# Optimization experiments

Hardware: AMD Instinct MI355X
Metric: run time of the kernel (lower is better)

The kernel has to match this reference:

```python
import jax, jax.numpy as jnp
import numpy as np

T, B, E = 2048, 16, 1024   # time, batch, embed_dim (fairseq T x B x C layout)
CDIM = 1024                # conv_dim
H = 16                     # num_heads
K = 31                     # kernel_size, padding_l = K-1 (causal left pad)


def _xavier(k, shape):
    fan_out, fan_in = shape
    lim = float(np.sqrt(6.0 / (fan_in + fan_out)))
    return jax.random.uniform(k, shape, jnp.float32, -lim, lim)


def setup_inputs() -> dict:
    key = jax.random.key(0)
    ks = jax.random.split(key, 5)
    return {
        "x": jax.random.normal(ks[0], (T, B, E), jnp.float32),
        "w1": _xavier(ks[1], (CDIM, E)),
        "b1": jnp.zeros((CDIM,), jnp.float32),
        "ww": _xavier(ks[2], (H * K, CDIM)),  # DynamicConv weight_linear
        "bw": jnp.zeros((H * K,), jnp.float32),
        "w2": _xavier(ks[3], (E, CDIM)),
        "b2": jnp.zeros((E,), jnp.float32),
        "gamma": jnp.ones((E,), jnp.float32),
        "beta": jnp.zeros((E,), jnp.float32),
    }


def layer_norm(x, g, b, eps=1e-5):
    m = x.mean(-1, keepdims=True)
    v = ((x - m) ** 2).mean(-1, keepdims=True)
    return (x - m) * jax.lax.rsqrt(v + eps) * g + b


def dynamic_conv(h, ww, bw):
    # h: [T, B, C]; per-position softmax kernel weights shared across R=C/H channels per head
    Tn, Bn, C = h.shape
    R = C // H
    w = jax.nn.softmax((h @ ww.T + bw).reshape(Tn, Bn, H, K), axis=-1)  # [T,B,H,K]
    hp = jnp.pad(h.reshape(Tn, Bn, H, R), ((K - 1, 0), (0, 0), (0, 0), (0, 0)))
    # out[t] = sum_k w[t,:,:,k] * h[t + k - (K-1)]  (causal banded aggregation)
    acc = jnp.zeros((Tn, Bn, H, R), h.dtype)
    for k in range(K):  # fixed small kernel-size loop, not a data-dim loop
        acc = acc + w[:, :, :, k:k + 1] * hp[k:k + Tn]
    return acc.reshape(Tn, Bn, C)


def reference(x, w1, b1, ww, bw, w2, b2, gamma, beta):
    # eval mode: all dropouts are identity; normalize_before=False -> LN after residual
    h = x @ w1.T + b1            # linear1: [T,B,E] -> [T,B,CDIM]
    h = dynamic_conv(h, ww, bw)  # DynamicConv, weight_softmax=True, no conv bias
    h = h @ w2.T + b2            # linear2: back to embed_dim
    return layer_norm(x + h, gamma, beta)
```

## Files before the change

### kernel.cpp

```cpp
#include <hip/hip_runtime.h>

#define T_DIM 2048
#define B_DIM 16
#define E_DIM 1024
#define CD    1024
#define NH    16
#define KSZ   31
#define M_DIM 32768
#define SLICE 131072
#define BSTRIDE 2097152

typedef unsigned int u32;
typedef unsigned short u16;
typedef __attribute__((ext_vector_type(8))) __bf16 bf16x8;
typedef __attribute__((ext_vector_type(4))) float f32x4;
typedef __attribute__((ext_vector_type(4))) float fvec4;
typedef __attribute__((ext_vector_type(8))) unsigned short us8;
typedef __attribute__((ext_vector_type(4))) unsigned short us4;
typedef __attribute__((ext_vector_type(4))) unsigned int ui4;

__device__ __forceinline__ float bf2f(u16 u) {
  union { float f; u32 i; } c; c.i = ((u32)u) << 16; return c.f;
}
__device__ __forceinline__ u16 f2bf(float f) {
  union { float f; u32 i; } c; c.f = f;
  u32 u = c.i;
  u += 0x7fffu + ((u >> 16) & 1u);
  return (u16)(u >> 16);
}

#define GLDS(gp, lp)                                                        \
  __builtin_amdgcn_global_load_lds(                                         \
      (__attribute__((address_space(1))) void*)(gp),                        \
      (__attribute__((address_space(3))) void*)(lp), 16, 0, 0)

__global__ __launch_bounds__(256) void zfill(u16* __restrict__ z) {
  ((ui4*)z)[threadIdx.x] = (ui4)(0u);
}

__global__ __launch_bounds__(256) void cvt_f32_bf16(const float* __restrict__ src,
                                                    u16* __restrict__ dst, int n4) {
  int i = blockIdx.x * 256 + threadIdx.x;
  int stride = gridDim.x * 256;
  const fvec4* s4 = (const fvec4*)src;
  us4* d4 = (us4*)dst;
  for (; i < n4; i += stride) {
    fvec4 v = s4[i];
    us4 o;
    o[0] = f2bf(v[0]); o[1] = f2bf(v[1]); o[2] = f2bf(v[2]); o[3] = f2bf(v[3]);
    d4[i] = o;
  }
}

__global__ __launch_bounds__(256) void cvt_x_tr(const float* __restrict__ x,
                                                u16* __restrict__ xbt) {
  int rr = blockIdx.x;
  int t = rr >> 4, b = rr & 15;
  const fvec4* src = (const fvec4*)(x + (size_t)rr * E_DIM);
  us4* dst = (us4*)(xbt + ((size_t)b * T_DIM + t) * E_DIM);
  fvec4 v = src[threadIdx.x];
  us4 o;
  o[0] = f2bf(v[0]); o[1] = f2bf(v[1]); o[2] = f2bf(v[2]); o[3] = f2bf(v[3]);
  dst[threadIdx.x] = o;
}

template<int OUT_MODE, int GUARD_N, int A_CONV>
__global__ __launch_bounds__(512, 2) void gemm256(
    const u16* __restrict__ A, const u16* __restrict__ B,
    const float* __restrict__ bias, void* __restrict__ Cout,
    int N, int K, int ldc, int ntn)
{
  __shared__ u16 sA[2][256 * 64];
  __shared__ u16 sB[2][256 * 64];
  const int tid = threadIdx.x;
  const int lane = tid & 63;
  const int wid = tid >> 6;
  const int wr = wid >> 2;
  const int wc = wid & 3;

  const int swz = (blockIdx.x & 7) * (gridDim.x >> 3) + (blockIdx.x >> 3);
  const int bm = (swz / ntn) * 256;
  const int bn = (swz % ntn) * 256;

  const int srow = tid >> 3;
  const int scol = (tid & 7) * 8;
  const int scols = scol ^ ((srow & 7) << 3);

  const u16* gA[4];
  #pragma unroll
  for (int st = 0; st < 4; st++) {
    int rr = bm + st * 64 + srow;
    if (A_CONV)
      gA[st] = A + (size_t)(rr >> 11) * BSTRIDE + (size_t)(rr & 2047) * 64 + scols;
    else
      gA[st] = A + (size_t)rr * K + scols;
  }
  const u16* gB[4];
  #pragma unroll
  for (int st = 0; st < 4; st++) {
    int br = bn + st * 64 + srow;
    if (GUARD_N) br = min(br, N - 1);
    gB[st] = B + (size_t)br * K + scols;
  }
  const int sdst = (tid >> 3) * 64 + scol;

  f32x4 acc[8][4];
  #pragma unroll
  for (int i = 0; i < 8; i++)
    #pragma unroll
    for (int j = 0; j < 4; j++) acc[i][j] = (f32x4)(0.0f);

  const int fr = lane & 15;
  const int g8 = (lane >> 4) * 8;
  const int sx = (fr & 7) << 3;

  const int NT = K >> 6;
  int buf = 0;

  #pragma unroll
  for (int st = 0; st < 4; st++) GLDS(gA[st], &sA[0][st * 4096 + sdst]);
  #pragma unroll
  for (int st = 0; st < 4; st++) GLDS(gB[st], &sB[0][st * 4096 + sdst]);
  asm volatile("s_waitcnt vmcnt(0)" ::: "memory");
  __builtin_amdgcn_s_barrier();

  for (int kt = 0; kt < NT; kt++) {
    bf16x8 bF[4][2];
    #pragma unroll
    for (int n = 0; n < 4; n++)
      #pragma unroll
      for (int kh = 0; kh < 2; kh++) {
        int row = wc * 64 + n * 16 + fr;
        bF[n][kh] = *(const bf16x8*)&sB[buf][row * 64 + ((kh * 32 + g8) ^ sx)];
      }
    bf16x8 aF[2][2];
    #pragma unroll
    for (int mi = 0; mi < 2; mi++)
      #pragma unroll
      for (int kh = 0; kh < 2; kh++) {
        int row = wr * 128 + mi * 16 + fr;
        aF[mi][kh] = *(const bf16x8*)&sA[buf][row * 64 + ((kh * 32 + g8) ^ sx)];
      }
    if (kt + 1 < NT) {
      const size_t koA = A_CONV ? (size_t)(kt + 1) * SLICE : (size_t)(kt + 1) * 64;
      const size_t koB = (size_t)(kt + 1) * 64;
      u16* dA = &sA[buf ^ 1][0];
      u16* dB = &sB[buf ^ 1][0];
      #pragma unroll
      for (int st = 0; st < 4; st++) GLDS(gA[st] + koA, dA + st * 4096 + sdst);
      #pragma unroll
      for (int st = 0; st < 4; st++) GLDS(gB[st] + koB, dB + st * 4096 + sdst);
    }
    __builtin_amdgcn_s_barrier();
    asm volatile("s_waitcnt lgkmcnt(0)" ::: "memory");
    __builtin_amdgcn_sched_barrier(0);
    __builtin_amdgcn_s_setprio(1);
    #pragma unroll
    for (int mi = 0; mi < 2; mi++)
      #pragma unroll
      for (int n = 0; n < 4; n++)
        #pragma unroll
        for (int kh = 0; kh < 2; kh++)
          acc[mi][n] = __builtin_amdgcn_mfma_f32_16x16x32_bf16(aF[mi][kh], bF[n][kh], acc[mi][n], 0, 0, 0);
    __builtin_amdgcn_s_setprio(0);
    __builtin_amdgcn_sched_barrier(0);
    __builtin_amdgcn_s_barrier();

    #pragma unroll
    for (int p = 1; p < 4; p++) {
      bf16x8 aG[2][2];
      #pragma unroll
      for (int mi = 0; mi < 2; mi++)
        #pragma unroll
        for (int kh = 0; kh < 2; kh++) {
          int row = wr * 128 + (2 * p + mi) * 16 + fr;
          aG[mi][kh] = *(const bf16x8*)&sA[buf][row * 64 + ((kh * 32 + g8) ^ sx)];
        }
      __builtin_amdgcn_s_barrier();
      asm volatile("s_waitcnt lgkmcnt(0)" ::: "memory");
      __builtin_amdgcn_sched_barrier(0);
      __builtin_amdgcn_s_setprio(1);
      #pragma unroll
      for (int mi = 0; mi < 2; mi++)
        #pragma unroll
        for (int n = 0; n < 4; n++)
          #pragma unroll
          for (int kh = 0; kh < 2; kh++)
            acc[2 * p + mi][n] = __builtin_amdgcn_mfma_f32_16x16x32_bf16(aG[mi][kh], bF[n][kh], acc[2 * p + mi][n], 0, 0, 0);
      __builtin_amdgcn_s_setprio(0);
      __builtin_amdgcn_sched_barrier(0);
      if (p < 3) {
        __builtin_amdgcn_s_barrier();
      } else {
        asm volatile("s_waitcnt vmcnt(0)" ::: "memory");
        __builtin_amdgcn_s_barrier();
      }
    }
    buf ^= 1;
  }

  const int orow0 = bm + wr * 128 + (lane >> 4) * 4;
  const int ocol0 = bn + wc * 64 + fr;
  #pragma unroll
  for (int m = 0; m < 8; m++) {
    #pragma unroll
    for (int n = 0; n < 4; n++) {
      #pragma unroll
      for (int q = 0; q < 4; q++) {
        int row = orow0 + m * 16 + q;
        int col = ocol0 + n * 16;
        if (!GUARD_N || col < N) {
          float v = acc[m][n][q] + bias[col];
          if (OUT_MODE == 1) {
            ((u16*)Cout)[(size_t)row * ldc + col] = f2bf(v);
          } else if (OUT_MODE == 2) {
            int bb = row >> 11, t = row & 2047;
            int hh = col / 31, kk = col - hh * 31;
            ((float*)Cout)[((size_t)((bb * NH + hh) * T_DIM + t)) * 32 + kk] = v;
          } else {
            int bb = row >> 11, t = row & 2047;
            ((u16*)Cout)[(size_t)((bb << 4) + (col >> 6)) * SLICE + (size_t)t * 64 + (col & 63)] = f2bf(v);
          }
        }
      }
    }
  }
}

__global__ __launch_bounds__(256) void softmax31(float* __restrict__ wt) {
  int idx = blockIdx.x * 256 + threadIdx.x;
  float* p = wt + (size_t)idx * 32;
  float v[KSZ];
  float mx = -1e30f;
  #pragma unroll
  for (int k = 0; k < KSZ; k++) { v[k] = p[k]; mx = fmaxf(mx, v[k]); }
  float s = 0.f;
  #pragma unroll
  for (int k = 0; k < KSZ; k++) { v[k] = __expf(v[k] - mx); s += v[k]; }
  float inv = 1.0f / s;
  #pragma unroll
  for (int k = 0; k < KSZ; k++) p[k] = v[k] * inv;
}

__global__ __launch_bounds__(256) void dconv(const u16* __restrict__ h1,
                                             const float* __restrict__ wt,
                                             const u16* __restrict__ zreg,
                                             u16* __restrict__ outc)
{
  constexpr int TT = 64, HALO = 30, SW = 33;
  int bid = blockIdx.x;
  int tt = bid & 31;
  int s  = bid >> 5;
  int t0 = tt * TT;
  __shared__ u16 hl[96 * 64];
  __shared__ float wl[TT * SW];
  int tid = threadIdx.x;

  const u16* slice = h1 + (size_t)s * SLICE;
  #pragma unroll
  for (int it = 0; it < 3; it++) {
    int c = it * 256 + tid;
    int row = t0 - HALO + (c >> 3);
    const u16* src = slice + (size_t)row * 64 + (c & 7) * 8;
    if (row < 0) src = zreg + (c & 7) * 8;
    GLDS(src, hl + c * 8);
  }
  const float* wsrc = wt + ((size_t)s * T_DIM + t0) * 32;
  #pragma unroll
  for (int it = 0; it < 2; it++) {
    int j = it * 1024 + tid * 4;
    f32x4 v = *(const f32x4*)(wsrc + j);
    int row = j >> 5, col = j & 31;
    *(f32x4*)(&wl[row * SW + col]) = v;
  }
  __syncthreads();

  int rb = (tid & 7) * 8;
  int tl = tid >> 3;

  #pragma unroll
  for (int half = 0; half < 2; half++) {
    const int tb = tl + half * 32;
    const float* wp = wl + tb * SW;
    const u16* hb = hl + tb * 64 + rb;
    float acc[8];
    #pragma unroll
    for (int e = 0; e < 8; e++) acc[e] = 0.f;
    #pragma unroll
    for (int k = 0; k < KSZ; k++) {
      us8 hv = *(const us8*)(hb + k * 64);
      float w = wp[k];
      #pragma unroll
      for (int e = 0; e < 8; e++) acc[e] += w * bf2f(hv[e]);
    }
    us8 o;
    #pragma unroll
    for (int e = 0; e < 8; e++) o[e] = f2bf(acc[e]);
    *(us8*)(outc + (size_t)s * SLICE + (size_t)(t0 + tb) * 64 + rb) = o;
  }
}

__global__ __launch_bounds__(256) void ln_res(const float* __restrict__ x,
                                              const u16* __restrict__ hb,
                                              float* __restrict__ out,
                                              const float* __restrict__ gamma,
                                              const float* __restrict__ beta)
{
  int mp = blockIdx.x;
  int b = mp >> 11, t = mp & 2047;
  int xrow = t * 16 + b;
  const fvec4* xr = (const fvec4*)(x + (size_t)xrow * E_DIM);
  const us4* hr = (const us4*)(hb + (size_t)mp * E_DIM);
  fvec4* yr = (fvec4*)(out + (size_t)xrow * E_DIM);
  int tid = threadIdx.x;
  us4 hv = hr[tid];
  fvec4 xv = xr[tid];
  fvec4 s;
  #pragma unroll
  for (int e = 0; e < 4; e++) s[e] = xv[e] + bf2f(hv[e]);
  float sum = s[0] + s[1] + s[2] + s[3];
  float sq  = s[0]*s[0] + s[1]*s[1] + s[2]*s[2] + s[3]*s[3];
  #pragma unroll
  for (int off = 32; off >= 1; off >>= 1) {
    sum += __shfl_xor(sum, off, 64);
    sq  += __shfl_xor(sq, off, 64);
  }
  __shared__ float red[8];
  int lane = tid & 63, wid = tid >> 6;
  if (lane == 0) { red[wid] = sum; red[4 + wid] = sq; }
  __syncthreads();
  sum = red[0] + red[1] + red[2] + red[3];
  sq  = red[4] + red[5] + red[6] + red[7];
  float mean = sum * (1.0f / E_DIM);
  float var  = sq * (1.0f / E_DIM) - mean * mean;
  float rstd = rsqrtf(var + 1e-5f);
  fvec4 g = ((const fvec4*)gamma)[tid];
  fvec4 be = ((const fvec4*)beta)[tid];
  fvec4 o;
  #pragma unroll
  for (int e = 0; e < 4; e++) o[e] = (s[e] - mean) * rstd * g[e] + be[e];
  yr[tid] = o;
}

extern "C" void kernel_launch(void* const* d_in, const int* in_sizes, int n_in,
                              void* d_out, int out_size, void* d_ws, size_t ws_size,
                              hipStream_t stream)
{
  const float* x     = (const float*)d_in[0];
  const float* w1    = (const float*)d_in[1];
  const float* b1    = (const float*)d_in[2];
  const float* ww    = (const float*)d_in[3];
  const float* bw    = (const float*)d_in[4];
  const float* w2    = (const float*)d_in[5];
  const float* b2    = (const float*)d_in[6];
  const float* gamma = (const float*)d_in[7];
  const float* beta  = (const float*)d_in[8];
  float* out = (float*)d_out;

  char* ws = (char*)d_ws;
  u16*   xbt  = (u16*)(ws);
  u16*   h1p  = (u16*)(ws + ((size_t)64 << 20));
  float* wt   = (float*)(ws + ((size_t)128 << 20));
  u16*   w1b  = (u16*)(ws + ((size_t)192 << 20));
  u16*   w2b  = (u16*)(ws + ((size_t)194 << 20));
  u16*   wwb  = (u16*)(ws + ((size_t)196 << 20));
  u16*   zreg = (u16*)(ws + ((size_t)198 << 20));
  u16*   convp = xbt;
  u16*   h2p  = h1p;

  zfill<<<1, 256, 0, stream>>>(zreg);
  cvt_x_tr<<<32768, 256, 0, stream>>>(x, xbt);
  cvt_f32_bf16<<<1024, 256, 0, stream>>>(w1, w1b, (CD * E_DIM) / 4);
  cvt_f32_bf16<<<1024, 256, 0, stream>>>(w2, w2b, (E_DIM * CD) / 4);
  cvt_f32_bf16<<<512,  256, 0, stream>>>(ww, wwb, (NH * KSZ * CD) / 4);

  gemm256<3, 0, 0><<<512, 512, 0, stream>>>(xbt, w1b, b1, h1p, CD, E_DIM, 0, 4);
  gemm256<2, 1, 1><<<256, 512, 0, stream>>>(h1p, wwb, bw, wt, NH * KSZ, CD, 0, 2);
  softmax31<<<2048, 256, 0, stream>>>(wt);
  dconv<<<8192, 256, 0, stream>>>(h1p, wt, zreg, convp);
  gemm256<1, 0, 1><<<512, 512, 0, stream>>>(convp, w2b, b2, h2p, E_DIM, CD, E_DIM, 4);
  ln_res<<<32768, 256, 0, stream>>>(x, h2p, out, gamma, beta);
}
```

Before: 424.1 us.

## Fuse softmax into dconv and split GEMM A-tile prefetch across phases

The separate softmax31 kernel is removed. Each dconv block now normalizes its 64 rows of kernel weights in shared memory, using 64 threads, after loading them. This saves one launch and a full read-write pass over the weight tensor, at the cost of a small serial stage and an extra barrier in dconv. In the GEMM, the next-tile global-to-LDS loads are now staggered: the B tile and half of the A tile are issued first, and the rest of A is issued after the second phase. Partial vmcnt waits replace the full drain, so memory traffic overlaps more with the MFMA phases.

```diff
diff --git a/kernel.cpp b/kernel.cpp
--- a/kernel.cpp
+++ b/kernel.cpp
@@ -118,13 +118,21 @@
   int buf = 0;
 
   #pragma unroll
-  for (int st = 0; st < 4; st++) GLDS(gA[st], &sA[0][st * 4096 + sdst]);
-  #pragma unroll
   for (int st = 0; st < 4; st++) GLDS(gB[st], &sB[0][st * 4096 + sdst]);
+  GLDS(gA[0], &sA[0][0 * 4096 + sdst]);
+  GLDS(gA[2], &sA[0][2 * 4096 + sdst]);
+  GLDS(gA[1], &sA[0][1 * 4096 + sdst]);
+  GLDS(gA[3], &sA[0][3 * 4096 + sdst]);
   asm volatile("s_waitcnt vmcnt(0)" ::: "memory");
   __builtin_amdgcn_s_barrier();
 
   for (int kt = 0; kt < NT; kt++) {
+    const bool more = (kt + 1 < NT);
+    const size_t koA = A_CONV ? (size_t)(kt + 1) * SLICE : (size_t)(kt + 1) * 64;
+    const size_t koB = (size_t)(kt + 1) * 64;
+    u16* dA = &sA[buf ^ 1][0];
+    u16* dB = &sB[buf ^ 1][0];
+
     bf16x8 bF[4][2];
     #pragma unroll
     for (int n = 0; n < 4; n++)
@@ -141,15 +149,13 @@
         int row = wr * 128 + mi * 16 + fr;
         aF[mi][kh] = *(const bf16x8*)&sA[buf][row * 64 + ((kh * 32 + g8) ^ sx)];
       }
-    if (kt + 1 < NT) {
-      const size_t koA = A_CONV ? (size_t)(kt + 1) * SLICE : (size_t)(kt + 1) * 64;
-      const size_t koB = (size_t)(kt + 1) * 64;
-      u16* dA = &sA[buf ^ 1][0];
-      u16* dB = &sB[buf ^ 1][0];
-      #pragma unroll
-      for (int st = 0; st < 4; st++) GLDS(gA[st] + koA, dA + st * 4096 + sdst);
-      #pragma unroll
-      for (int st = 0; st < 4; st++) GLDS(gB[st] + koB, dB + st * 4096 + sdst);
+    if (more) {
+      GLDS(gB[0] + koB, dB + 0 * 4096 + sdst);
+      GLDS(gB[1] + koB, dB + 1 * 4096 + sdst);
+      GLDS(gB[2] + koB, dB + 2 * 4096 + sdst);
+      GLDS(gB[3] + koB, dB + 3 * 4096 + sdst);
+      GLDS(gA[0] + koA, dA + 0 * 4096 + sdst);
+      GLDS(gA[2] + koA, dA + 2 * 4096 + sdst);
     }
     __builtin_amdgcn_s_barrier();
     asm volatile("s_waitcnt lgkmcnt(0)" ::: "memory");
@@ -176,6 +182,10 @@
           int row = wr * 128 + (2 * p + mi) * 16 + fr;
           aG[mi][kh] = *(const bf16x8*)&sA[buf][row * 64 + ((kh * 32 + g8) ^ sx)];
         }
+      if (p == 1 && more) {
+        GLDS(gA[1] + koA, dA + 1 * 4096 + sdst);
+        GLDS(gA[3] + koA, dA + 3 * 4096 + sdst);
+      }
       __builtin_amdgcn_s_barrier();
       asm volatile("s_waitcnt lgkmcnt(0)" ::: "memory");
       __builtin_amdgcn_sched_barrier(0);
@@ -189,12 +199,14 @@
             acc[2 * p + mi][n] = __builtin_amdgcn_mfma_f32_16x16x32_bf16(aG[mi][kh], bF[n][kh], acc[2 * p + mi][n], 0, 0, 0);
       __builtin_amdgcn_s_setprio(0);
       __builtin_amdgcn_sched_barrier(0);
-      if (p < 3) {
-        __builtin_amdgcn_s_barrier();
-      } else {
-        asm volatile("s_waitcnt vmcnt(0)" ::: "memory");
-        __builtin_amdgcn_s_barrier();
-      }
+      if (p == 1) {
+        if (more) { asm volatile("s_waitcnt vmcnt(8)" ::: "memory"); }
+        else      { asm volatile("s_waitcnt vmcnt(0)" ::: "memory"); }
+      }
+      if (p == 3 && more) {
+        asm volatile("s_waitcnt vmcnt(2)" ::: "memory");
+      }
+      __builtin_amdgcn_s_barrier();
     }
     buf ^= 1;
   }
@@ -227,21 +239,6 @@
   }
 }
 
-__global__ __launch_bounds__(256) void softmax31(float* __restrict__ wt) {
-  int idx = blockIdx.x * 256 + threadIdx.x;
-  float* p = wt + (size_t)idx * 32;
-  float v[KSZ];
-  float mx = -1e30f;
-  #pragma unroll
-  for (int k = 0; k < KSZ; k++) { v[k] = p[k]; mx = fmaxf(mx, v[k]); }
-  float s = 0.f;
-  #pragma unroll
-  for (int k = 0; k < KSZ; k++) { v[k] = __expf(v[k] - mx); s += v[k]; }
-  float inv = 1.0f / s;
-  #pragma unroll
-  for (int k = 0; k < KSZ; k++) p[k] = v[k] * inv;
-}
-
 __global__ __launch_bounds__(256) void dconv(const u16* __restrict__ h1,
                                              const float* __restrict__ wt,
                                              const u16* __restrict__ zreg,
@@ -272,6 +269,21 @@
     f32x4 v = *(const f32x4*)(wsrc + j);
     int row = j >> 5, col = j & 31;
     *(f32x4*)(&wl[row * SW + col]) = v;
+  }
+  __syncthreads();
+
+  if (tid < TT) {
+    float* p = wl + tid * SW;
+    float v[KSZ];
+    float mx = -1e30f;
+    #pragma unroll
+    for (int k = 0; k < KSZ; k++) { v[k] = p[k]; mx = fmaxf(mx, v[k]); }
+    float sum = 0.f;
+    #pragma unroll
+    for (int k = 0; k < KSZ; k++) { v[k] = __expf(v[k] - mx); sum += v[k]; }
+    float inv = 1.0f / sum;
+    #pragma unroll
+    for (int k = 0; k < KSZ; k++) p[k] = v[k] * inv;
   }
   __syncthreads();
 
@@ -376,7 +388,6 @@
 
   gemm256<3, 0, 0><<<512, 512, 0, stream>>>(xbt, w1b, b1, h1p, CD, E_DIM, 0, 4);
   gemm256<2, 1, 1><<<256, 512, 0, stream>>>(h1p, wwb, bw, wt, NH * KSZ, CD, 0, 2);
-  softmax31<<<2048, 256, 0, stream>>>(wt);
   dconv<<<8192, 256, 0, stream>>>(h1p, wt, zreg, convp);
   gemm256<1, 0, 1><<<512, 512, 0, stream>>>(convp, w2b, b2, h2p, E_DIM, CD, E_DIM, 4);
   ln_res<<<32768, 256, 0, stream>>>(x, h2p, out, gamma, beta);
```

Result: faster. 384.1 us (-9.4%).
